# Kernel tuning notes

Hardware: AMD Instinct MI355X
Metric: run time of the kernel (lower is better)

The kernel has to match this reference:

```python
import jax, jax.numpy as jnp
import numpy as np

DIM = 768
HEADS = 12
HEAD_DIM = DIM // HEADS
SCALE = HEAD_DIM ** -0.5
LN_EPS = 1e-5


def setup_inputs() -> dict:
    key = jax.random.key(0)
    ks = jax.random.split(key, 12)
    B, N, C = 8, 1024, DIM
    g = (6.0 / (C + 3 * C)) ** 0.5  # xavier_uniform bound for qkv
    gp = (6.0 / (C + C)) ** 0.5     # xavier_uniform bound for proj
    return {
        "x": jax.random.normal(ks[0], (B, N, C), jnp.float32),
        "w_qkv_id": jax.random.uniform(ks[1], (3 * C, C), jnp.float32, -g, g),
        "w_qkv_cloth": jax.random.uniform(ks[2], (3 * C, C), jnp.float32, -g, g),
        "w_proj_id": jax.random.uniform(ks[3], (C, C), jnp.float32, -gp, gp),
        "b_proj_id": jnp.zeros((C,), jnp.float32),
        "w_proj_cloth": jax.random.uniform(ks[4], (C, C), jnp.float32, -gp, gp),
        "b_proj_cloth": jnp.zeros((C,), jnp.float32),
        "ln_id_w": jnp.ones((C,), jnp.float32),
        "ln_id_b": jnp.zeros((C,), jnp.float32),
        "ln_cloth_w": jnp.ones((C,), jnp.float32),
        "ln_cloth_b": jnp.zeros((C,), jnp.float32),
        "orth_scale": jnp.asarray(0.1, jnp.float32),
    }


def _layernorm(x, w, b):
    mu = jnp.mean(x, axis=-1, keepdims=True)
    var = jnp.var(x, axis=-1, keepdims=True)
    return (x - mu) * jax.lax.rsqrt(var + LN_EPS) * w + b


def _split_heads(qkv, B, N):
    qkv = qkv.reshape(B, N, 3, HEADS, HEAD_DIM).transpose(2, 0, 3, 1, 4)
    return qkv[0], qkv[1], qkv[2]


def _attn(q, k, v):
    s = jnp.einsum("bhnd,bhmd->bhnm", q, k) * SCALE
    s = jnp.clip(s, -20.0, 20.0)
    a = jax.nn.softmax(s, axis=-1)
    a = jnp.where(jnp.isnan(a), jnp.zeros_like(a), a)  # nan guard (dropout = eval/identity)
    return jnp.einsum("bhnm,bhmd->bhnd", a, v)


def reference(x, w_qkv_id, w_qkv_cloth, w_proj_id, b_proj_id, w_proj_cloth,
              b_proj_cloth, ln_id_w, ln_id_b, ln_cloth_w, ln_cloth_b, orth_scale):
    B, N, C = x.shape
    q_id, k_id, v_id = _split_heads(x @ w_qkv_id.T, B, N)
    q_cl, k_cl, v_cl = _split_heads(x @ w_qkv_cloth.T, B, N)

    # Gram-Schmidt orthogonal projection of q_id against q_cloth
    dot = jnp.sum(q_id * q_cl, axis=-1, keepdims=True)          # [B,H,N,1]
    norm_sq = jnp.sum(q_cl * q_cl, axis=-1, keepdims=True) + 1e-5
    coeff = jnp.clip(dot / norm_sq, -1.0, 1.0)
    scale = jnp.clip(orth_scale, 0.0, 1.0)
    q_id_ortho = q_id - scale * (coeff * q_cl)
    saliency = jnp.clip(jnp.mean(jnp.abs(dot) / jnp.sqrt(norm_sq), axis=1), 0.0, 1.0)  # [B,N,1]

    out_id = _attn(q_id_ortho, k_id, v_id).transpose(0, 2, 1, 3).reshape(B, N, C)
    out_cl = _attn(q_cl, k_cl, v_cl).transpose(0, 2, 1, 3).reshape(B, N, C)

    id_feat = _layernorm(out_id @ w_proj_id.T + b_proj_id, ln_id_w, ln_id_b)
    cl_feat = _layernorm(out_cl @ w_proj_cloth.T + b_proj_cloth, ln_cloth_w, ln_cloth_b)
    return id_feat, cl_feat, saliency
```

## Files before the change

### kernel.cpp

```cpp
#include <hip/hip_runtime.h>

typedef unsigned short u16;
typedef short s16x8 __attribute__((ext_vector_type(8)));
typedef float f32x4 __attribute__((ext_vector_type(4)));

#define DEV __device__ __forceinline__

#if __has_builtin(__builtin_amdgcn_exp2f)
#define EXP2F(x) __builtin_amdgcn_exp2f(x)
#else
#define EXP2F(x) exp2f(x)
#endif

DEV u16 f2bf(float f) {
  unsigned int u = __float_as_uint(f);
  u = (u + 0x7fffu + ((u >> 16) & 1u)) >> 16;
  return (u16)u;
}
DEV float bf2f(u16 h) { return __uint_as_float(((unsigned int)h) << 16); }
DEV unsigned int pk_trunc(float lo, float hi) {
  return __builtin_amdgcn_perm(__float_as_uint(hi), __float_as_uint(lo), 0x07060302u);
}

DEV void g2l16(const void* g, void* l) {
  __builtin_amdgcn_global_load_lds(
      (const __attribute__((address_space(1))) unsigned int*)g,
      (__attribute__((address_space(3))) unsigned int*)l, 16, 0, 0);
}

#define SPLANE 6291456

#define BAR __builtin_amdgcn_s_barrier()
#define WAIT_VM(n) asm volatile("s_waitcnt vmcnt(" #n ")" ::: "memory")
#define WAIT_LGKM0 asm volatile("s_waitcnt lgkmcnt(0)" ::: "memory")
#define PRIO1 __builtin_amdgcn_s_setprio(1)
#define PRIO0 __builtin_amdgcn_s_setprio(0)

__global__ __launch_bounds__(256) void k_cvt(const float* __restrict__ x,
                                             const float* __restrict__ wqi,
                                             const float* __restrict__ wqc,
                                             const float* __restrict__ wpi,
                                             const float* __restrict__ wpc,
                                             u16* __restrict__ xb,
                                             u16* __restrict__ wqkv,
                                             u16* __restrict__ wproj) {
  int i = blockIdx.x * 256 + threadIdx.x;
  const float* src; u16* dst; int off;
  if (i < 1572864)      { src = x;   dst = xb;             off = 0; }
  else if (i < 2015232) { src = wqi; dst = wqkv;           off = 1572864; }
  else if (i < 2457600) { src = wqc; dst = wqkv + 1769472; off = 2015232; }
  else if (i < 2605056) { src = wpi; dst = wproj;          off = 2457600; }
  else                  { src = wpc; dst = wproj + 589824; off = 2605056; }
  int j = i - off;
  float4 v = ((const float4*)src)[j];
  ushort4 o;
  o.x = f2bf(v.x); o.y = f2bf(v.y); o.z = f2bf(v.z); o.w = f2bf(v.w);
  ((ushort4*)dst)[j] = o;
}


DEV void qstg(const u16* pX, const u16* pW, int koff, u16* lA, u16* lB, int wave) {
#pragma unroll
  for (int it = 0; it < 4; ++it) {
    int rb = wave * 32 + it * 8;
    g2l16(pX + koff + it * (8 * 768), &lA[rb * 64]);
    g2l16(pW + koff + it * (8 * 768), &lB[rb * 64]);
  }
}

DEV void qcomp(const u16* lA, const u16* lB, int wr, int wc, int fr, int fq,
               f32x4 (&acc)[4][4]) {
#pragma unroll
  for (int ks = 0; ks < 2; ++ks) {
    s16x8 af[4], bfr[4];
#pragma unroll
    for (int i = 0; i < 4; i++) {
      int row = wc + i * 16 + fr;
      af[i] = *(const s16x8*)&lB[row * 64 + (((ks * 4 + fq) ^ (row & 7)) * 8)];
    }
#pragma unroll
    for (int j = 0; j < 4; j++) {
      int row = wr + j * 16 + fr;
      bfr[j] = *(const s16x8*)&lA[row * 64 + (((ks * 4 + fq) ^ (row & 7)) * 8)];
    }
    PRIO1;
#pragma unroll
    for (int i = 0; i < 4; i++)
#pragma unroll
      for (int j = 0; j < 4; j++)
        acc[i][j] = __builtin_amdgcn_mfma_f32_16x16x32_bf16(af[i], bfr[j], acc[i][j], 0, 0, 0);
    PRIO0;
  }
}

__global__ __launch_bounds__(256, 2) void k_qkv_gemm(const u16* __restrict__ X,
                                                     const u16* __restrict__ Wq,
                                                     u16* __restrict__ QK,
                                                     u16* __restrict__ VT,
                                                     float* __restrict__ sal) {
  __shared__ __align__(16) u16 sm[32768];

  const int idx = blockIdx.x;
  const int tid = threadIdx.x;
  if (idx < 32) sal[idx * 256 + tid] = 0.f;

  const int swz = (idx & 7) * 288 + (idx >> 3);
  const int bx = swz % 18;
  const int rem = swz / 18;
  const int by = rem & 63;
  const int z = rem >> 6;
  const int n0 = bx * 128, m0 = by * 128;

  const int wave = tid >> 6, lane = tid & 63;
  const int wr = (wave >> 1) * 64, wc = (wave & 1) * 64;
  const int fr = lane & 15, fq = lane >> 4;

  const int srow = lane >> 3;
  const int scol = ((lane & 7) ^ srow) * 8;

  const u16* pX = X + (size_t)(m0 + wave * 32 + srow) * 768 + scol;
  const u16* pW = Wq + (size_t)z * (2304 * 768) + (size_t)(n0 + wave * 32 + srow) * 768 + scol;

  u16* const lA0 = sm;
  u16* const lB0 = sm + 8192;
  u16* const lA1 = sm + 16384;
  u16* const lB1 = sm + 24576;

  f32x4 acc[4][4];
#pragma unroll
  for (int i = 0; i < 4; i++)
#pragma unroll
    for (int j = 0; j < 4; j++) acc[i][j] = (f32x4){0.f, 0.f, 0.f, 0.f};

  qstg(pX, pW, 0, lA0, lB0, wave);
  qstg(pX, pW, 64, lA1, lB1, wave);
  WAIT_VM(8);
  BAR;

  const u16* pX2 = pX + 128;
  const u16* pW2 = pW + 128;

#pragma unroll
  for (int ii = 0; ii < 6; ++ii) {
    qcomp(lA0, lB0, wr, wc, fr, fq, acc);
    BAR;
    if (ii < 5) {
      qstg(pX2, pW2, 0, lA0, lB0, wave);
      WAIT_VM(8);
    } else {
      WAIT_VM(0);
    }
    BAR;
    qcomp(lA1, lB1, wr, wc, fr, fq, acc);
    BAR;
    if (ii < 5) {
      qstg(pX2, pW2, 64, lA1, lB1, wave);
      WAIT_VM(8);
      pX2 += 128; pW2 += 128;
    }
    BAR;
  }

  __syncthreads();
  const int c0 = n0 + wc;
  const int t0 = m0 + wr;
  const int b = t0 >> 10, tt0 = t0 & 1023;
  if (c0 < 1536) {
    u16* ep = sm + wave * 4608;
#pragma unroll
    for (int i = 0; i < 4; i++)
#pragma unroll
      for (int j = 0; j < 4; j++) {
        unsigned int lo = (unsigned int)f2bf(acc[i][j][0]) | ((unsigned int)f2bf(acc[i][j][1]) << 16);
        unsigned int hi = (unsigned int)f2bf(acc[i][j][2]) | ((unsigned int)f2bf(acc[i][j][3]) << 16);
        uint2 pk; pk.x = lo; pk.y = hi;
        *(uint2*)&ep[(j * 16 + fr) * 72 + i * 16 + fq * 4] = pk;
      }
    __builtin_amdgcn_s_waitcnt(0);
    const int three = (c0 >= 768) ? 1 : 0;
    const int h = (c0 - three * 768) >> 6;
    u16* dst = QK + ((size_t)z * 2 + three) * SPLANE +
               ((size_t)(b * 12 + h) * 1024 + tt0) * 64;
#pragma unroll
    for (int pass = 0; pass < 8; ++pass) {
      int row = pass * 8 + (lane >> 3);
      int dch = (lane & 7) * 8;
      *(uint4*)&dst[(size_t)row * 64 + dch] = *(const uint4*)&ep[row * 72 + dch];
    }
  } else {
    const int h = (c0 - 1536) >> 6;
    u16* dst = VT + (size_t)z * SPLANE + ((size_t)(b * 12 + h) * 64) * 1024 + tt0;
    u16* ep2 = sm + wave * 5632;
#pragma unroll
    for (int i = 0; i < 4; i++)
#pragma unroll
      for (int j = 0; j < 4; j++)
#pragma unroll
        for (int r = 0; r < 4; r++)
          ep2[(i * 16 + fq * 4 + r) * 88 + j * 16 + fr] = f2bf(acc[i][j][r]);
    __builtin_amdgcn_s_waitcnt(0);
#pragma unroll
    for (int pass = 0; pass < 8; ++pass) {
      int d = pass * 8 + (lane >> 3);
      int tch = (lane & 7) * 8;
      *(uint4*)&dst[(size_t)d * 1024 + tch] = *(const uint4*)&ep2[d * 88 + tch];
    }
  }
}

#define AST 72
#define PST 40
__global__ __launch_bounds__(256, 3) void k_attn(const u16* __restrict__ QK,
                                                 const u16* __restrict__ VT,
                                                 const float* __restrict__ orth_scale,
                                                 float* __restrict__ sal,
                                                 u16* __restrict__ aout) {
  __shared__ __align__(16) u16 sm[19456];
  u16* lK = sm;
  u16* lVT = sm + 4608;
  const int lid = blockIdx.x;
  const int swz = (lid & 7) * 96 + (lid >> 3);
  const int qb = swz & 3;
  const int pr = swz >> 2;
  const int z = pr / 96, bh = pr - (pr / 96) * 96;
  const int q0 = qb * 256;
  const int b = bh / 12, hd = bh - b * 12;
  const size_t plane = (size_t)bh * 65536;
  const u16* Q  = QK + (size_t)z * 2 * SPLANE + plane;
  const u16* K  = QK + ((size_t)z * 2 + 1) * SPLANE + plane;
  const u16* Vt = VT + (size_t)z * SPLANE + plane;

  const int tid = threadIdx.x, wave = tid >> 6, lane = tid & 63;
  const int fr = lane & 15, fq = lane >> 4;
  u16* lP = sm + 9216 + wave * 2560;

  s16x8 qf[4][2];
#pragma unroll
  for (int s = 0; s < 4; s++) {
    const u16* qrow = Q + (size_t)(q0 + wave * 64 + s * 16 + fr) * 64;
    qf[s][0] = *(const s16x8*)&qrow[fq * 8];
    qf[s][1] = *(const s16x8*)&qrow[32 + fq * 8];
  }

  if (z == 0) {
    const float scale = fminf(fmaxf(orth_scale[0], 0.f), 1.f);
    const u16* Qc = QK + (size_t)2 * SPLANE + plane;
#pragma unroll
    for (int s = 0; s < 4; s++) {
      const u16* qcrow = Qc + (size_t)(q0 + wave * 64 + s * 16 + fr) * 64;
      s16x8 qc0 = *(const s16x8*)&qcrow[fq * 8];
      s16x8 qc1 = *(const s16x8*)&qcrow[32 + fq * 8];
      float d = 0.f, nq = 0.f;
#pragma unroll
      for (int e = 0; e < 8; e++) {
        float a0 = bf2f((u16)qf[s][0][e]), a1 = bf2f((u16)qf[s][1][e]);
        float c0 = bf2f((u16)qc0[e]),      c1 = bf2f((u16)qc1[e]);
        d  = fmaf(a0, c0, fmaf(a1, c1, d));
        nq = fmaf(c0, c0, fmaf(c1, c1, nq));
      }
      d += __shfl_xor(d, 16);  d += __shfl_xor(d, 32);
      nq += __shfl_xor(nq, 16); nq += __shfl_xor(nq, 32);
      nq += 1e-5f;
      float coeff = fminf(fmaxf(d / nq, -1.f), 1.f);
      float sc = scale * coeff;
#pragma unroll
      for (int e = 0; e < 8; e++) {
        qf[s][0][e] = (short)f2bf(bf2f((u16)qf[s][0][e]) - sc * bf2f((u16)qc0[e]));
        qf[s][1][e] = (short)f2bf(bf2f((u16)qf[s][1][e]) - sc * bf2f((u16)qc1[e]));
      }
      if (lane < 16)
        atomicAdd(&sal[b * 1024 + q0 + wave * 64 + s * 16 + fr], fabsf(d) / sqrtf(nq));
    }
  }

  f32x4 oacc[4][4];
  float lsum[4];
#pragma unroll
  for (int s = 0; s < 4; s++) {
    lsum[s] = 0.f;
#pragma unroll
    for (int j = 0; j < 4; j++) oacc[s][j] = (f32x4){0.f, 0.f, 0.f, 0.f};
  }

  const int srow = tid >> 3, sc8 = (tid & 7) * 8;

  uint4 rk0 = *(const uint4*)&K[(size_t)srow * 64 + sc8];
  uint4 rk1 = *(const uint4*)&K[(size_t)(srow + 32) * 64 + sc8];
  uint4 rv0 = *(const uint4*)&Vt[(size_t)srow * 1024 + sc8];
  uint4 rv1 = *(const uint4*)&Vt[(size_t)(srow + 32) * 1024 + sc8];

  for (int kv0 = 0; kv0 < 1024; kv0 += 64) {
    __syncthreads();
    *(uint4*)&lK[srow * AST + sc8]         = rk0;
    *(uint4*)&lK[(srow + 32) * AST + sc8]  = rk1;
    *(uint4*)&lVT[srow * AST + sc8]        = rv0;
    *(uint4*)&lVT[(srow + 32) * AST + sc8] = rv1;
    __syncthreads();

    {
      int nxt = (kv0 + 64) & 1023;
      const u16* kb = K + (size_t)nxt * 64;
      rk0 = *(const uint4*)&kb[(size_t)srow * 64 + sc8];
      rk1 = *(const uint4*)&kb[(size_t)(srow + 32) * 64 + sc8];
      const u16* vb = Vt + nxt;
      rv0 = *(const uint4*)&vb[(size_t)srow * 1024 + sc8];
      rv1 = *(const uint4*)&vb[(size_t)(srow + 32) * 1024 + sc8];
    }

#pragma unroll
    for (int ph = 0; ph < 2; ++ph) {
#pragma unroll
      for (int jh = 0; jh < 2; ++jh) {
        const int jt = ph * 2 + jh;
        s16x8 kf0 = *(const s16x8*)&lK[(jt * 16 + fr) * AST + fq * 8];
        s16x8 kf1 = *(const s16x8*)&lK[(jt * 16 + fr) * AST + 32 + fq * 8];
#pragma unroll
        for (int s = 0; s < 4; s++) {
          f32x4 t = (f32x4){0.f, 0.f, 0.f, 0.f};
          t = __builtin_amdgcn_mfma_f32_16x16x32_bf16(kf0, qf[s][0], t, 0, 0, 0);
          t = __builtin_amdgcn_mfma_f32_16x16x32_bf16(kf1, qf[s][1], t, 0, 0, 0);
          float p0 = EXP2F(fmaf(t[0], 0.18033688f, -28.8539008f));
          float p1 = EXP2F(fmaf(t[1], 0.18033688f, -28.8539008f));
          float p2 = EXP2F(fmaf(t[2], 0.18033688f, -28.8539008f));
          float p3 = EXP2F(fmaf(t[3], 0.18033688f, -28.8539008f));
          lsum[s] += (p0 + p1) + (p2 + p3);
          uint2 pk; pk.x = pk_trunc(p0, p1); pk.y = pk_trunc(p2, p3);
          *(uint2*)&lP[(s * 16 + fr) * PST + jh * 16 + fq * 4] = pk;
        }
      }
      WAIT_LGKM0;
      s16x8 pa[4];
#pragma unroll
      for (int s = 0; s < 4; s++) pa[s] = *(const s16x8*)&lP[(s * 16 + fr) * PST + fq * 8];
#pragma unroll
      for (int jt = 0; jt < 4; jt++) {
        s16x8 vb = *(const s16x8*)&lVT[(jt * 16 + fr) * AST + ph * 32 + fq * 8];
#pragma unroll
        for (int s = 0; s < 4; s++)
          oacc[s][jt] = __builtin_amdgcn_mfma_f32_16x16x32_bf16(pa[s], vb, oacc[s][jt], 0, 0, 0);
      }
    }
  }

#pragma unroll
  for (int s = 0; s < 4; s++) {
    float v = lsum[s];
    v += __shfl_xor(v, 16);
    v += __shfl_xor(v, 32);
    lsum[s] = v;
  }
#pragma unroll
  for (int s = 0; s < 4; s++) {
#pragma unroll
    for (int r = 0; r < 4; r++) {
      float inv = 1.f / __shfl(lsum[s], fq * 4 + r);
      int t = q0 + wave * 64 + s * 16 + fq * 4 + r;
      size_t base = ((size_t)z * 8192 + b * 1024 + t) * 768 + hd * 64 + fr;
#pragma unroll
      for (int jt = 0; jt < 4; jt++)
        aout[base + jt * 16] = f2bf(oacc[s][jt][r] * inv);
    }
  }
}

__global__ __launch_bounds__(256) void k_proj_gemm(const u16* __restrict__ A,
                                                   const u16* __restrict__ Wp,
                                                   const float* __restrict__ bias_id,
                                                   const float* __restrict__ bias_cl,
                                                   float* __restrict__ sal,
                                                   u16* __restrict__ out) {
  __shared__ __align__(16) u16 sm[18432];
  u16* lA = sm;
  u16* lB = sm + 8192;
  const int idx = blockIdx.x;
  const int tid = threadIdx.x;
  if (idx < 32) {
    int i2 = idx * 256 + tid;
    float v = sal[i2] * (1.f / 12.f);
    sal[i2] = fminf(fmaxf(v, 0.f), 1.f);
  }
  const int swz = (idx & 7) * 96 + (idx >> 3);
  const int bx = swz % 6;
  const int rem = swz / 6;
  const int by = rem & 63;
  const int z = rem >> 6;
  const int n0 = bx * 128, m0 = by * 128;
  const u16* Az = A + (size_t)z * 8192 * 768;
  const u16* Wz = Wp + (size_t)z * 768 * 768;
  const float* bias = z ? bias_cl : bias_id;
  u16* oz = out + (size_t)z * 8192 * 768;
  const int wave = tid >> 6, lane = tid & 63;
  const int wr = (wave >> 1) * 64, wc = (wave & 1) * 64;
  const int fr = lane & 15, fq = lane >> 4;

  float bv[4][4];
#pragma unroll
  for (int i = 0; i < 4; i++)
#pragma unroll
    for (int r = 0; r < 4; r++) bv[i][r] = bias[n0 + wc + i * 16 + fq * 4 + r];

  f32x4 acc[4][4];
#pragma unroll
  for (int i = 0; i < 4; i++)
#pragma unroll
    for (int j = 0; j < 4; j++) acc[i][j] = (f32x4){0.f, 0.f, 0.f, 0.f};

  const int srow = lane >> 3;
  const int scol = ((lane & 7) ^ srow) * 8;

  const u16* pAz = Az + (size_t)(m0 + wave * 32 + srow) * 768 + scol;
  const u16* pWz = Wz + (size_t)(n0 + wave * 32 + srow) * 768 + scol;

  for (int k0 = 0; k0 < 768; k0 += 64) {
    __syncthreads();
#pragma unroll
    for (int it = 0; it < 4; ++it) {
      int rb = wave * 32 + it * 8;
      g2l16(pAz + it * (8 * 768) + k0, &lA[rb * 64]);
      g2l16(pWz + it * (8 * 768) + k0, &lB[rb * 64]);
    }
    __syncthreads();
#pragma unroll
    for (int ks = 0; ks < 2; ++ks) {
      s16x8 af[4], bfr[4];
#pragma unroll
      for (int i = 0; i < 4; i++) {
        int row = wc + i * 16 + fr;
        af[i] = *(const s16x8*)&lB[row * 64 + (((ks * 4 + fq) ^ (row & 7)) * 8)];
      }
#pragma unroll
      for (int j = 0; j < 4; j++) {
        int row = wr + j * 16 + fr;
        bfr[j] = *(const s16x8*)&lA[row * 64 + (((ks * 4 + fq) ^ (row & 7)) * 8)];
      }
#pragma unroll
      for (int i = 0; i < 4; i++)
#pragma unroll
        for (int j = 0; j < 4; j++)
          acc[i][j] = __builtin_amdgcn_mfma_f32_16x16x32_bf16(af[i], bfr[j], acc[i][j], 0, 0, 0);
    }
  }

  __syncthreads();
  u16* ep = sm + wave * 4608;
#pragma unroll
  for (int i = 0; i < 4; i++)
#pragma unroll
    for (int j = 0; j < 4; j++) {
      unsigned int lo = (unsigned int)f2bf(acc[i][j][0] + bv[i][0]) |
                        ((unsigned int)f2bf(acc[i][j][1] + bv[i][1]) << 16);
      unsigned int hi = (unsigned int)f2bf(acc[i][j][2] + bv[i][2]) |
                        ((unsigned int)f2bf(acc[i][j][3] + bv[i][3]) << 16);
      uint2 pk; pk.x = lo; pk.y = hi;
      *(uint2*)&ep[(j * 16 + fr) * 72 + i * 16 + fq * 4] = pk;
    }
  __builtin_amdgcn_s_waitcnt(0);

  const int c0 = n0 + wc;
#pragma unroll
  for (int pass = 0; pass < 8; ++pass) {
    int row = pass * 8 + (lane >> 3);
    int dch = (lane & 7) * 8;
    u16* dst = oz + (size_t)(m0 + wr + row) * 768 + c0;
    *(uint4*)&dst[dch] = *(const uint4*)&ep[row * 72 + dch];
  }
}

__global__ __launch_bounds__(256) void k_ln(const u16* __restrict__ pin,
                                            const float* __restrict__ w_id,
                                            const float* __restrict__ b_id,
                                            const float* __restrict__ w_cl,
                                            const float* __restrict__ b_cl,
                                            float* __restrict__ out) {
  __shared__ float red[2][8];
  const int row = blockIdx.x;
  const int z = row >> 13;
  const float* w = z ? w_cl : w_id;
  const float* bb = z ? b_cl : b_id;
  const u16* x = pin + (size_t)row * 768;
  float v[3];
  float s = 0.f, s2 = 0.f;
#pragma unroll
  for (int i = 0; i < 3; i++) {
    v[i] = bf2f(x[threadIdx.x + i * 256]);
    s += v[i];
    s2 += v[i] * v[i];
  }
#pragma unroll
  for (int sh = 1; sh < 64; sh <<= 1) { s += __shfl_xor(s, sh); s2 += __shfl_xor(s2, sh); }
  const int wave = threadIdx.x >> 6, lane = threadIdx.x & 63;
  if (lane == 0) { red[0][wave] = s; red[1][wave] = s2; }
  __syncthreads();
  s = red[0][0] + red[0][1] + red[0][2] + red[0][3];
  s2 = red[1][0] + red[1][1] + red[1][2] + red[1][3];
  float mu = s * (1.f / 768.f);
  float var = s2 * (1.f / 768.f) - mu * mu;
  float rstd = rsqrtf(fmaxf(var, 0.f) + 1e-5f);
  float* o = out + (size_t)row * 768;
#pragma unroll
  for (int i = 0; i < 3; i++) {
    int c = threadIdx.x + i * 256;
    o[c] = (v[i] - mu) * rstd * w[c] + bb[c];
  }
}

extern "C" void kernel_launch(void* const* d_in, const int* in_sizes, int n_in,
                              void* d_out, int out_size, void* d_ws, size_t ws_size,
                              hipStream_t stream) {
  const float* x        = (const float*)d_in[0];
  const float* w_qkv_id = (const float*)d_in[1];
  const float* w_qkv_cl = (const float*)d_in[2];
  const float* w_proj_id= (const float*)d_in[3];
  const float* b_proj_id= (const float*)d_in[4];
  const float* w_proj_cl= (const float*)d_in[5];
  const float* b_proj_cl= (const float*)d_in[6];
  const float* ln_id_w  = (const float*)d_in[7];
  const float* ln_id_b  = (const float*)d_in[8];
  const float* ln_cl_w  = (const float*)d_in[9];
  const float* ln_cl_b  = (const float*)d_in[10];
  const float* orth     = (const float*)d_in[11];
  float* out = (float*)d_out;
  float* sal = out + 12582912;

  u16* xb    = (u16*)d_ws;
  u16* wqkv  = xb + 6291456;
  u16* wproj = wqkv + 3538944;
  u16* qk    = wproj + 1179648;
  u16* vt    = qk + 25165824;
  u16* aout  = vt + 12582912;
  u16* pout  = qk;

  k_cvt<<<10752, 256, 0, stream>>>(x, w_qkv_id, w_qkv_cl, w_proj_id, w_proj_cl,
                                   xb, wqkv, wproj);
  k_qkv_gemm<<<2304, 256, 0, stream>>>(xb, wqkv, qk, vt, sal);
  k_attn<<<768, 256, 0, stream>>>(qk, vt, orth, sal, aout);
  k_proj_gemm<<<768, 256, 0, stream>>>(aout, wproj, b_proj_id, b_proj_cl, sal, pout);
  k_ln<<<16384, 256, 0, stream>>>(pout, ln_id_w, ln_id_b, ln_cl_w, ln_cl_b, out);
}
```

Measured before the change: 279.1 us.

## Fold softmax scale into Q epilogue and double-buffer projection GEMM loads

```diff
diff --git a/kernel.cpp b/kernel.cpp
--- a/kernel.cpp
+++ b/kernel.cpp
@@ -29,6 +29,7 @@
 }
 
 #define SPLANE 6291456
+#define QSCALE 0.18033688f
 
 #define BAR __builtin_amdgcn_s_barrier()
 #define WAIT_VM(n) asm volatile("s_waitcnt vmcnt(" #n ")" ::: "memory")
@@ -166,13 +167,16 @@
   const int t0 = m0 + wr;
   const int b = t0 >> 10, tt0 = t0 & 1023;
   if (c0 < 1536) {
+    const float qs = (c0 < 768) ? QSCALE : 1.0f;
     u16* ep = sm + wave * 4608;
 #pragma unroll
     for (int i = 0; i < 4; i++)
 #pragma unroll
       for (int j = 0; j < 4; j++) {
-        unsigned int lo = (unsigned int)f2bf(acc[i][j][0]) | ((unsigned int)f2bf(acc[i][j][1]) << 16);
-        unsigned int hi = (unsigned int)f2bf(acc[i][j][2]) | ((unsigned int)f2bf(acc[i][j][3]) << 16);
+        unsigned int lo = (unsigned int)f2bf(acc[i][j][0] * qs) |
+                          ((unsigned int)f2bf(acc[i][j][1] * qs) << 16);
+        unsigned int hi = (unsigned int)f2bf(acc[i][j][2] * qs) |
+                          ((unsigned int)f2bf(acc[i][j][3] * qs) << 16);
         uint2 pk; pk.x = lo; pk.y = hi;
         *(uint2*)&ep[(j * 16 + fr) * 72 + i * 16 + fq * 4] = pk;
       }
@@ -260,7 +264,7 @@
       }
       d += __shfl_xor(d, 16);  d += __shfl_xor(d, 32);
       nq += __shfl_xor(nq, 16); nq += __shfl_xor(nq, 32);
-      nq += 1e-5f;
+      nq += 3.25214e-7f;
       float coeff = fminf(fmaxf(d / nq, -1.f), 1.f);
       float sc = scale * coeff;
 #pragma unroll
@@ -319,10 +323,10 @@
           f32x4 t = (f32x4){0.f, 0.f, 0.f, 0.f};
           t = __builtin_amdgcn_mfma_f32_16x16x32_bf16(kf0, qf[s][0], t, 0, 0, 0);
           t = __builtin_amdgcn_mfma_f32_16x16x32_bf16(kf1, qf[s][1], t, 0, 0, 0);
-          float p0 = EXP2F(fmaf(t[0], 0.18033688f, -28.8539008f));
-          float p1 = EXP2F(fmaf(t[1], 0.18033688f, -28.8539008f));
-          float p2 = EXP2F(fmaf(t[2], 0.18033688f, -28.8539008f));
-          float p3 = EXP2F(fmaf(t[3], 0.18033688f, -28.8539008f));
+          float p0 = EXP2F(t[0]);
+          float p1 = EXP2F(t[1]);
+          float p2 = EXP2F(t[2]);
+          float p3 = EXP2F(t[3]);
           lsum[s] += (p0 + p1) + (p2 + p3);
           uint2 pk; pk.x = pk_trunc(p0, p1); pk.y = pk_trunc(p2, p3);
           *(uint2*)&lP[(s * 16 + fr) * PST + jh * 16 + fq * 4] = pk;
@@ -363,20 +367,18 @@
   }
 }
 
-__global__ __launch_bounds__(256) void k_proj_gemm(const u16* __restrict__ A,
-                                                   const u16* __restrict__ Wp,
-                                                   const float* __restrict__ bias_id,
-                                                   const float* __restrict__ bias_cl,
-                                                   float* __restrict__ sal,
-                                                   u16* __restrict__ out) {
-  __shared__ __align__(16) u16 sm[18432];
-  u16* lA = sm;
-  u16* lB = sm + 8192;
+__global__ __launch_bounds__(256, 2) void k_proj_gemm(const u16* __restrict__ A,
+                                                      const u16* __restrict__ Wp,
+                                                      const float* __restrict__ bias_id,
+                                                      const float* __restrict__ bias_cl,
+                                                      float* __restrict__ sal,
+                                                      u16* __restrict__ out) {
+  __shared__ __align__(16) u16 sm[32768];
   const int idx = blockIdx.x;
   const int tid = threadIdx.x;
   if (idx < 32) {
     int i2 = idx * 256 + tid;
-    float v = sal[i2] * (1.f / 12.f);
+    float v = sal[i2] * 0.46209812f;
     sal[i2] = fminf(fmaxf(v, 0.f), 1.f);
   }
   const int swz = (idx & 7) * 96 + (idx >> 3);
@@ -411,34 +413,38 @@
   const u16* pAz = Az + (size_t)(m0 + wave * 32 + srow) * 768 + scol;
   const u16* pWz = Wz + (size_t)(n0 + wave * 32 + srow) * 768 + scol;
 
-  for (int k0 = 0; k0 < 768; k0 += 64) {
-    __syncthreads();
-#pragma unroll
-    for (int it = 0; it < 4; ++it) {
-      int rb = wave * 32 + it * 8;
-      g2l16(pAz + it * (8 * 768) + k0, &lA[rb * 64]);
-      g2l16(pWz + it * (8 * 768) + k0, &lB[rb * 64]);
-    }
-    __syncthreads();
-#pragma unroll
-    for (int ks = 0; ks < 2; ++ks) {
-      s16x8 af[4], bfr[4];
-#pragma unroll
-      for (int i = 0; i < 4; i++) {
-        int row = wc + i * 16 + fr;
-        af[i] = *(const s16x8*)&lB[row * 64 + (((ks * 4 + fq) ^ (row & 7)) * 8)];
-      }
-#pragma unroll
-      for (int j = 0; j < 4; j++) {
-        int row = wr + j * 16 + fr;
-        bfr[j] = *(const s16x8*)&lA[row * 64 + (((ks * 4 + fq) ^ (row & 7)) * 8)];
-      }
-#pragma unroll
-      for (int i = 0; i < 4; i++)
-#pragma unroll
-        for (int j = 0; j < 4; j++)
-          acc[i][j] = __builtin_amdgcn_mfma_f32_16x16x32_bf16(af[i], bfr[j], acc[i][j], 0, 0, 0);
-    }
+  u16* const lA0 = sm;
+  u16* const lB0 = sm + 8192;
+  u16* const lA1 = sm + 16384;
+  u16* const lB1 = sm + 24576;
+
+  qstg(pAz, pWz, 0, lA0, lB0, wave);
+  qstg(pAz, pWz, 64, lA1, lB1, wave);
+  WAIT_VM(8);
+  BAR;
+
+  const u16* pA2 = pAz + 128;
+  const u16* pW2 = pWz + 128;
+
+#pragma unroll
+  for (int ii = 0; ii < 6; ++ii) {
+    qcomp(lA0, lB0, wr, wc, fr, fq, acc);
+    BAR;
+    if (ii < 5) {
+      qstg(pA2, pW2, 0, lA0, lB0, wave);
+      WAIT_VM(8);
+    } else {
+      WAIT_VM(0);
+    }
+    BAR;
+    qcomp(lA1, lB1, wr, wc, fr, fq, acc);
+    BAR;
+    if (ii < 5) {
+      qstg(pA2, pW2, 64, lA1, lB1, wave);
+      WAIT_VM(8);
+      pA2 += 128; pW2 += 128;
+    }
+    BAR;
   }
 
   __syncthreads();
```

After: 289.2 us. 3.6% more time.
